# Kernel optimization log

Hardware: AMD Instinct MI355X
Metric: run time of the kernel (lower is better)

## Reference

```python
import jax, jax.numpy as jnp
import numpy as np

B, T, D_MODEL, D_HIDDEN = 4, 8192, 1024, 1024
EPS = 1e-5

def setup_inputs() -> dict:
    key = jax.random.key(0)
    ks = jax.random.split(key, 8)
    s_in = 1.0 / np.sqrt(D_MODEL)
    s_h = 1.0 / np.sqrt(D_HIDDEN)
    return {
        "x": jax.random.normal(ks[0], (B, T, D_MODEL), jnp.float32),
        "W_ih": jax.random.uniform(ks[1], (D_MODEL, D_HIDDEN), jnp.float32, -s_in, s_in),
        "b_ih": jnp.zeros((D_HIDDEN,), jnp.float32),
        "W_gate": jax.random.uniform(ks[2], (D_MODEL, D_HIDDEN), jnp.float32, -s_in, s_in),
        "b_gate": jnp.zeros((D_HIDDEN,), jnp.float32),
        "log_a": jnp.full((D_HIDDEN,), -0.1, jnp.float32),
        "ln_g": jnp.ones((D_HIDDEN,), jnp.float32),
        "ln_b": jnp.zeros((D_HIDDEN,), jnp.float32),
        "W_out": jax.random.uniform(ks[3], (D_HIDDEN, D_HIDDEN), jnp.float32, -s_h, s_h),
        "b_out": jnp.zeros((D_HIDDEN,), jnp.float32),
        "W_proj": jax.random.uniform(ks[4], (D_HIDDEN, D_MODEL), jnp.float32, -s_h, s_h),
        "b_proj": jnp.zeros((D_MODEL,), jnp.float32),
    }

def _scan(alpha, beta):
    # h_t = alpha_t * h_{t-1} + beta_t, h_0 = 0, over axis 1 (time)
    def combine(c1, c2):
        a1, b1 = c1
        a2, b2 = c2
        return a2 * a1, a2 * b1 + b2
    _, h = jax.lax.associative_scan(combine, (alpha, beta), axis=1)
    return h

def reference(x, W_ih, b_ih, W_gate, b_gate, log_a, ln_g, ln_b, W_out, b_out, W_proj, b_proj):
    ih = jnp.einsum("btd,dh->bth", x, W_ih) + b_ih
    gate = jax.nn.sigmoid(jnp.einsum("btd,dh->bth", x, W_gate) + b_gate)
    a = jnp.exp(log_a)  # [H]
    alpha = (1.0 - gate) * a  # [B,T,H]
    beta = gate * ih
    h = _scan(alpha, beta)
    # LayerNorm over last dim
    mu = jnp.mean(h, axis=-1, keepdims=True)
    var = jnp.var(h, axis=-1, keepdims=True)
    hn = (h - mu) * jax.lax.rsqrt(var + EPS) * ln_g + ln_b
    out = jnp.einsum("bth,ho->bto", hn, W_out) + b_out
    return jnp.einsum("bth,hd->btd", out, W_proj) + b_proj
```

## Files before the change

kernel.cpp:

```cpp
#include <hip/hip_runtime.h>

typedef short bhalf8 __attribute__((ext_vector_type(8)));
typedef float floatx4 __attribute__((ext_vector_type(4)));
typedef unsigned short ushortx8 __attribute__((ext_vector_type(8)));

__device__ __forceinline__ unsigned short f2bf(float f){
  union { float f; unsigned int u; } v; v.f = f;
  unsigned int u = v.u;
  u += 0x7fffu + ((u >> 16) & 1u);
  return (unsigned short)(u >> 16);
}
__device__ __forceinline__ float bf2f(unsigned short u){
  union { unsigned int u; float f; } v; v.u = ((unsigned)u) << 16; return v.f;
}
__device__ __forceinline__ unsigned pack2(float a, float b){
  return (unsigned)f2bf(a) | ((unsigned)f2bf(b) << 16);
}

__device__ __forceinline__ void async16(const unsigned short* g, unsigned short* l){
  __builtin_amdgcn_global_load_lds(
      (const __attribute__((address_space(1))) void*)g,
      (__attribute__((address_space(3))) void*)l,
      16, 0, 0);
}

template<int EPI>
__global__ __launch_bounds__(256) void gemm_k(
    const unsigned short* __restrict__ Ab, const unsigned short* __restrict__ BT,
    const float* __restrict__ bias, float* __restrict__ Cf,
    unsigned short* __restrict__ Cb, int K, int ldc)
{
  __shared__ __align__(16) unsigned short As[128*64];
  __shared__ __align__(16) unsigned short Bs[128*64];
  const int tid = threadIdx.x;
  const int n0 = blockIdx.x * 128;
  const int m0 = blockIdx.y * 128;
  const int wid = tid >> 6, lane = tid & 63;
  const int wr = (wid >> 1) * 64, wc = (wid & 1) * 64;
  const int r16 = lane & 15, quad = lane >> 4;
  const int ldsbase = (tid & ~63) * 8;

  const unsigned short* pA[4];
  const unsigned short* pB[4];
  #pragma unroll
  for (int i = 0; i < 4; ++i) {
    int p = tid + i*256;
    int row = p >> 3;
    int cp = (p & 7) ^ (row & 7);
    pA[i] = Ab + (size_t)(m0+row)*K + cp*8;
    pB[i] = BT + (size_t)(n0+row)*K + cp*8;
  }
  int aoff[2][4], boff[2][4];
  #pragma unroll
  for (int ks = 0; ks < 2; ++ks){
    #pragma unroll
    for (int mi = 0; mi < 4; ++mi){
      int row = wr + mi*16 + r16;
      aoff[ks][mi] = (row*8 + ((ks*4+quad) ^ (row&7))) * 8;
    }
    #pragma unroll
    for (int ni = 0; ni < 4; ++ni){
      int row = wc + ni*16 + r16;
      boff[ks][ni] = (row*8 + ((ks*4+quad) ^ (row&7))) * 8;
    }
  }

  floatx4 acc[4][4];
  #pragma unroll
  for (int i=0;i<4;i++)
    #pragma unroll
    for (int j2=0;j2<4;j2++) acc[i][j2] = {0.f,0.f,0.f,0.f};

  for (int k0 = 0; k0 < K; k0 += 64) {
    #pragma unroll
    for (int i = 0; i < 4; ++i) async16(pA[i], &As[ldsbase + i*2048]);
    #pragma unroll
    for (int i = 0; i < 4; ++i) async16(pB[i], &Bs[ldsbase + i*2048]);
    __syncthreads();
    #pragma unroll
    for (int ks = 0; ks < 2; ++ks) {
      bhalf8 aF[4], bF[4];
      #pragma unroll
      for (int mi=0;mi<4;++mi) aF[mi] = *(const bhalf8*)&As[aoff[ks][mi]];
      #pragma unroll
      for (int ni=0;ni<4;++ni) bF[ni] = *(const bhalf8*)&Bs[boff[ks][ni]];
      #pragma unroll
      for (int mi=0;mi<4;++mi)
        #pragma unroll
        for (int ni=0;ni<4;++ni)
          acc[mi][ni] = __builtin_amdgcn_mfma_f32_16x16x32_bf16(aF[mi], bF[ni], acc[mi][ni], 0, 0, 0);
    }
    __syncthreads();
    #pragma unroll
    for (int i = 0; i < 4; ++i) { pA[i] += 64; pB[i] += 64; }
  }

  #pragma unroll
  for (int mi=0;mi<4;++mi)
    #pragma unroll
    for (int ni=0;ni<4;++ni)
      #pragma unroll
      for (int rr=0;rr<4;++rr){
        int m = m0 + wr + mi*16 + quad*4 + rr;
        int n = n0 + wc + ni*16 + r16;
        float val = acc[mi][ni][rr];
        if (EPI == 0) Cf[(size_t)m*ldc + n] = val;
        else if (EPI == 1) Cf[(size_t)m*ldc + n] = val + bias[n];
        else if (EPI == 3) Cb[(size_t)m*ldc + n] = f2bf(val + bias[n]);
        else Cb[(size_t)n*ldc + m] = f2bf(val);
      }
}

__global__ __launch_bounds__(256) void prep_all(
    const float* __restrict__ W_ih, const float* __restrict__ W_gate,
    const float* __restrict__ W_proj, const float* __restrict__ W_out,
    const float* __restrict__ b_out,
    const float* __restrict__ log_a, const float* __restrict__ b_ih,
    const float* __restrict__ b_gate, const float* __restrict__ x,
    unsigned short* __restrict__ WcatT, unsigned short* __restrict__ WprojT,
    unsigned short* __restrict__ Woutb, unsigned short* __restrict__ xb,
    float* __restrict__ Pc, float* __restrict__ a_vec, float* __restrict__ bcat)
{
  __shared__ float tile[32][33];
  const int blk = blockIdx.x;
  const int tid = threadIdx.x;
  if (blk < 3072) {
    const int which = blk >> 10;
    const int t = blk & 1023;
    const float* src = (which == 0) ? W_ih : (which == 1) ? W_gate : W_proj;
    unsigned short* dst = (which == 0) ? WcatT : (which == 1) ? (WcatT + 1024*1024) : WprojT;
    const int c0 = (t & 31) * 32, r0 = (t >> 5) * 32;
    const int tx = tid & 31, ty = tid >> 5;
    #pragma unroll
    for (int i = 0; i < 32; i += 8)
      tile[ty+i][tx] = src[(size_t)(r0+ty+i)*1024 + c0+tx];
    __syncthreads();
    #pragma unroll
    for (int i = 0; i < 32; i += 8)
      dst[(size_t)(c0+ty+i)*1024 + r0+tx] = f2bf(tile[tx][ty+i]);
  } else if (blk < 4096) {
    int idx = ((blk - 3072)*256 + tid) * 4;
    float4 v = *(const float4*)(W_out + idx);
    uint2 p;
    p.x = pack2(v.x, v.y);
    p.y = pack2(v.z, v.w);
    *(uint2*)(Woutb + idx) = p;
  } else if (blk < 4160) {
    int blk2 = blk - 4096;
    int dgrp = blk2 >> 4, seg = blk2 & 15;
    int d = dgrp*256 + tid;
    int e0 = seg*64;
    float acc = 0.f;
    #pragma unroll 8
    for (int e = 0; e < 64; ++e)
      acc += b_out[e0+e] * W_proj[(size_t)(e0+e)*1024 + d];
    Pc[seg*1024 + d] = acc;
  } else if (blk < 4168) {
    int d = (blk - 4160)*256 + tid;
    if (d < 1024) {
      a_vec[d] = __expf(log_a[d]);
      bcat[d] = b_ih[d];
    } else {
      bcat[d] = b_gate[d-1024];
    }
  } else {
    int idx = ((blk - 4168)*256 + tid) * 4;
    float4 v = *(const float4*)(x + idx);
    uint2 p;
    p.x = pack2(v.x, v.y);
    p.y = pack2(v.z, v.w);
    *(uint2*)(xb + idx) = p;
  }
}

#define CHUNK 16
#define NCHUNK 512

__device__ __forceinline__ void ab_step(unsigned short iu, unsigned short gu,
                                        float a, float& al, float& be)
{
  float zi = bf2f(iu), zg = bf2f(gu);
  float g = 1.f / (1.f + __expf(-zg));
  al = (1.f - g) * a;
  be = g * zi;
}

__global__ __launch_bounds__(256, 4) void scan_phase1(const unsigned short* __restrict__ pre,
    const float* __restrict__ a_vec, float* __restrict__ AsT, float* __restrict__ SsT)
{
  __shared__ float sA[4][1024];
  __shared__ float sS[4][1024];
  int wid = threadIdx.x >> 6, lane = threadIdx.x & 63;
  int u = blockIdx.x*4 + wid;
  int b = u >> 9, c = u & (NCHUNK-1);
  int ch0 = lane*16;
  float a[16], A[16], S[16];
  #pragma unroll
  for (int q=0;q<4;++q) *(float4*)&a[q*4] = *(const float4*)(a_vec + ch0 + q*4);
  #pragma unroll
  for (int j=0;j<16;++j){ A[j]=1.f; S[j]=0.f; }
  size_t base = ((size_t)(b*8192 + c*CHUNK))*2048 + ch0;
  for (int t=0;t<CHUNK;++t){
    ushortx8 i0 = *(const ushortx8*)(pre + base);
    ushortx8 i1 = *(const ushortx8*)(pre + base + 8);
    ushortx8 g0 = *(const ushortx8*)(pre + base + 1024);
    ushortx8 g1 = *(const ushortx8*)(pre + base + 1032);
    #pragma unroll
    for (int j=0;j<8;++j){
      float al, be;
      ab_step(i0[j], g0[j], a[j], al, be);
      A[j] *= al; S[j] = al*S[j] + be;
      ab_step(i1[j], g1[j], a[j+8], al, be);
      A[j+8] *= al; S[j+8] = al*S[j+8] + be;
    }
    base += 2048;
  }
  #pragma unroll
  for (int j=0;j<16;++j){ sA[wid][ch0+j] = A[j]; sS[wid][ch0+j] = S[j]; }
  __syncthreads();
  const int bb = blockIdx.x >> 7;
  const int c0 = (blockIdx.x*4) & (NCHUNK-1);
  const int t = threadIdx.x;
  #pragma unroll
  for (int q=0;q<4;++q){
    int ch = t + q*256;
    float4 va = make_float4(sA[0][ch], sA[1][ch], sA[2][ch], sA[3][ch]);
    float4 vs = make_float4(sS[0][ch], sS[1][ch], sS[2][ch], sS[3][ch]);
    size_t o = ((size_t)(bb*1024 + ch))*NCHUNK + c0;
    *(float4*)(AsT + o) = va;
    *(float4*)(SsT + o) = vs;
  }
}

__global__ __launch_bounds__(256) void scan_phase2(const float* __restrict__ AsT,
    const float* __restrict__ SsT, float* __restrict__ carryT,
    const float* __restrict__ Pc, const float* __restrict__ b_proj,
    float* __restrict__ b_comb)
{
  int wid = threadIdx.x >> 6, lane = threadIdx.x & 63;
  int p = blockIdx.x*4 + wid;
  size_t base = (size_t)p*NCHUNK + lane*8;
  float4 a0 = *(const float4*)(AsT + base);
  float4 a1 = *(const float4*)(AsT + base + 4);
  float4 s0 = *(const float4*)(SsT + base);
  float4 s1 = *(const float4*)(SsT + base + 4);
  float A = a0.x, S = s0.x;
  A = a0.y*A; S = a0.y*S + s0.y;
  A = a0.z*A; S = a0.z*S + s0.z;
  A = a0.w*A; S = a0.w*S + s0.w;
  A = a1.x*A; S = a1.x*S + s1.x;
  A = a1.y*A; S = a1.y*S + s1.y;
  A = a1.z*A; S = a1.z*S + s1.z;
  A = a1.w*A; S = a1.w*S + s1.w;
  float iA = A, iS = S;
  #pragma unroll
  for (int d = 1; d < 64; d <<= 1) {
    float pA = __shfl_up(iA, d);
    float pS = __shfl_up(iS, d);
    if (lane >= d) { iS = iA*pS + iS; iA = iA*pA; }
  }
  float bS = __shfl_up(iS, 1);
  if (lane == 0) bS = 0.f;
  float4 c0v, c1v;
  c0v.x = bS; bS = a0.x*bS + s0.x;
  c0v.y = bS; bS = a0.y*bS + s0.y;
  c0v.z = bS; bS = a0.z*bS + s0.z;
  c0v.w = bS; bS = a0.w*bS + s0.w;
  c1v.x = bS; bS = a1.x*bS + s1.x;
  c1v.y = bS; bS = a1.y*bS + s1.y;
  c1v.z = bS; bS = a1.z*bS + s1.z;
  c1v.w = bS;
  *(float4*)(carryT + base)     = c0v;
  *(float4*)(carryT + base + 4) = c1v;

  if (blockIdx.x == 0) {
    #pragma unroll
    for (int q = 0; q < 4; ++q) {
      int d = threadIdx.x + q*256;
      float acc = b_proj[d];
      #pragma unroll
      for (int s = 0; s < 16; ++s) acc += Pc[s*1024 + d];
      b_comb[d] = acc;
    }
  }
}

__global__ __launch_bounds__(256, 4) void scan_phase3(const unsigned short* __restrict__ pre,
    const float* __restrict__ a_vec, const float* __restrict__ carryT,
    const float* __restrict__ ln_g, const float* __restrict__ ln_b,
    unsigned short* __restrict__ hn)
{
  int wid = threadIdx.x >> 6, lane = threadIdx.x & 63;
  int u = blockIdx.x*4 + wid;
  int b = u >> 9, c = u & (NCHUNK-1);
  int ch0 = lane*16;
  float a[16], h[16], g[16], lb[16];
  #pragma unroll
  for (int q=0;q<4;++q){
    *(float4*)&a[q*4]  = *(const float4*)(a_vec + ch0 + q*4);
    *(float4*)&g[q*4]  = *(const float4*)(ln_g + ch0 + q*4);
    *(float4*)&lb[q*4] = *(const float4*)(ln_b + ch0 + q*4);
  }
  #pragma unroll
  for (int j=0;j<16;++j)
    h[j] = carryT[((size_t)b*1024 + ch0 + j)*NCHUNK + c];
  size_t base  = ((size_t)(b*8192 + c*CHUNK))*2048 + ch0;
  size_t hbase = ((size_t)(b*8192 + c*CHUNK))*1024 + ch0;
  for (int t=0;t<CHUNK;++t){
    ushortx8 i0 = *(const ushortx8*)(pre + base);
    ushortx8 i1 = *(const ushortx8*)(pre + base + 8);
    ushortx8 g0 = *(const ushortx8*)(pre + base + 1024);
    ushortx8 g1 = *(const ushortx8*)(pre + base + 1032);
    float s = 0.f, s2 = 0.f;
    #pragma unroll
    for (int j=0;j<8;++j){
      float al, be;
      ab_step(i0[j], g0[j], a[j], al, be);
      h[j] = al*h[j] + be;
      s += h[j]; s2 += h[j]*h[j];
      ab_step(i1[j], g1[j], a[j+8], al, be);
      h[j+8] = al*h[j+8] + be;
      s += h[j+8]; s2 += h[j+8]*h[j+8];
    }
    #pragma unroll
    for (int off = 32; off > 0; off >>= 1) {
      s  += __shfl_xor(s,  off);
      s2 += __shfl_xor(s2, off);
    }
    float mu = s * (1.f/1024.f);
    float var = s2 * (1.f/1024.f) - mu*mu;
    float rstd = rsqrtf(var + 1e-5f);
    uint4 o0, o1;
    float v0, v1;
    v0 = (h[0]-mu)*rstd*g[0]+lb[0];  v1 = (h[1]-mu)*rstd*g[1]+lb[1];  o0.x = pack2(v0,v1);
    v0 = (h[2]-mu)*rstd*g[2]+lb[2];  v1 = (h[3]-mu)*rstd*g[3]+lb[3];  o0.y = pack2(v0,v1);
    v0 = (h[4]-mu)*rstd*g[4]+lb[4];  v1 = (h[5]-mu)*rstd*g[5]+lb[5];  o0.z = pack2(v0,v1);
    v0 = (h[6]-mu)*rstd*g[6]+lb[6];  v1 = (h[7]-mu)*rstd*g[7]+lb[7];  o0.w = pack2(v0,v1);
    v0 = (h[8]-mu)*rstd*g[8]+lb[8];  v1 = (h[9]-mu)*rstd*g[9]+lb[9];  o1.x = pack2(v0,v1);
    v0 = (h[10]-mu)*rstd*g[10]+lb[10]; v1 = (h[11]-mu)*rstd*g[11]+lb[11]; o1.y = pack2(v0,v1);
    v0 = (h[12]-mu)*rstd*g[12]+lb[12]; v1 = (h[13]-mu)*rstd*g[13]+lb[13]; o1.z = pack2(v0,v1);
    v0 = (h[14]-mu)*rstd*g[14]+lb[14]; v1 = (h[15]-mu)*rstd*g[15]+lb[15]; o1.w = pack2(v0,v1);
    *(uint4*)(hn + hbase)     = o0;
    *(uint4*)(hn + hbase + 8) = o1;
    base += 2048; hbase += 1024;
  }
}

extern "C" void kernel_launch(void* const* d_in, const int* in_sizes, int n_in,
                              void* d_out, int out_size, void* d_ws, size_t ws_size,
                              hipStream_t stream)
{
  const float* x      = (const float*)d_in[0];
  const float* W_ih   = (const float*)d_in[1];
  const float* b_ih   = (const float*)d_in[2];
  const float* W_gate = (const float*)d_in[3];
  const float* b_gate = (const float*)d_in[4];
  const float* log_a  = (const float*)d_in[5];
  const float* ln_g   = (const float*)d_in[6];
  const float* ln_b   = (const float*)d_in[7];
  const float* W_out  = (const float*)d_in[8];
  const float* b_out  = (const float*)d_in[9];
  const float* W_proj = (const float*)d_in[10];
  const float* b_proj = (const float*)d_in[11];
  float* out = (float*)d_out;

  char* ws = (char*)d_ws;
  size_t off = 0;
  auto alloc = [&](size_t bytes)->char* {
    char* p = ws + off; off += (bytes + 255) & ~(size_t)255; return p;
  };
  unsigned short* pre   = (unsigned short*)alloc((size_t)32768*2048*2);
  unsigned short* hn    = (unsigned short*)alloc((size_t)32768*1024*2);
  unsigned short* xb    = hn;
  unsigned short* WcatT = (unsigned short*)alloc((size_t)2048*1024*2);
  unsigned short* WprojT= (unsigned short*)alloc((size_t)1024*1024*2);
  unsigned short* Woutb = (unsigned short*)alloc((size_t)1024*1024*2);
  unsigned short* WcombT= (unsigned short*)alloc((size_t)1024*1024*2);
  float* AsT            = (float*)alloc((size_t)4*1024*NCHUNK*4);
  float* SsT            = (float*)alloc((size_t)4*1024*NCHUNK*4);
  float* carryT         = (float*)alloc((size_t)4*1024*NCHUNK*4);
  float* Pc             = (float*)alloc((size_t)16*1024*4);
  float* b_comb         = (float*)alloc(1024*4);
  float* a_vec          = (float*)alloc(1024*4);
  float* bcat           = (float*)alloc(2048*4);

  prep_all<<<4168 + 32768, 256, 0, stream>>>(W_ih, W_gate, W_proj, W_out, b_out,
                                             log_a, b_ih, b_gate, x,
                                             WcatT, WprojT, Woutb, xb,
                                             Pc, a_vec, bcat);
  gemm_k<2><<<dim3(8,8), 256, 0, stream>>>(Woutb, WprojT, nullptr, nullptr, WcombT, 1024, 1024);
  gemm_k<3><<<dim3(16,256), 256, 0, stream>>>(xb, WcatT, bcat, nullptr, pre, 1024, 2048);
  scan_phase1<<<512, 256, 0, stream>>>(pre, a_vec, AsT, SsT);
  scan_phase2<<<1024, 256, 0, stream>>>(AsT, SsT, carryT, Pc, b_proj, b_comb);
  scan_phase3<<<512, 256, 0, stream>>>(pre, a_vec, carryT, ln_g, ln_b, hn);
  gemm_k<1><<<dim3(8,256), 256, 0, stream>>>(hn, WcombT, b_comb, out, nullptr, 1024, 1024);
}
```

Before: 618.5 us.

## Swap MFMA operands for vectorized GEMM epilogue, simplify address math, transpose carry layout

For the bias epilogues, the GEMM passes the MFMA operands in swapped order so each lane holds four consecutive output columns. This allows float4 and packed bf16x4 stores and float4 bias loads in place of scalar strided stores. LDS and global address computation is collapsed into a base offset plus XOR with the k-step, which reduces register pressure. The scan carry buffer is changed to a time-major layout so phase3 reads each carry with contiguous float4 loads instead of 16 strided scalar loads, while phase2 now issues strided scalar stores.

```diff
diff --git a/kernel.cpp b/kernel.cpp
--- a/kernel.cpp
+++ b/kernel.cpp
@@ -40,30 +40,15 @@
   const int r16 = lane & 15, quad = lane >> 4;
   const int ldsbase = (tid & ~63) * 8;
 
-  const unsigned short* pA[4];
-  const unsigned short* pB[4];
-  #pragma unroll
-  for (int i = 0; i < 4; ++i) {
-    int p = tid + i*256;
-    int row = p >> 3;
-    int cp = (p & 7) ^ (row & 7);
-    pA[i] = Ab + (size_t)(m0+row)*K + cp*8;
-    pB[i] = BT + (size_t)(n0+row)*K + cp*8;
-  }
-  int aoff[2][4], boff[2][4];
-  #pragma unroll
-  for (int ks = 0; ks < 2; ++ks){
-    #pragma unroll
-    for (int mi = 0; mi < 4; ++mi){
-      int row = wr + mi*16 + r16;
-      aoff[ks][mi] = (row*8 + ((ks*4+quad) ^ (row&7))) * 8;
-    }
-    #pragma unroll
-    for (int ni = 0; ni < 4; ++ni){
-      int row = wc + ni*16 + r16;
-      boff[ks][ni] = (row*8 + ((ks*4+quad) ^ (row&7))) * 8;
-    }
-  }
+  const int row0 = tid >> 3;
+  const int cp0  = (tid & 7) ^ (row0 & 7);
+  const unsigned short* pA0 = Ab + (size_t)(m0+row0)*K + cp0*8;
+  const unsigned short* pB0 = BT + (size_t)(n0+row0)*K + cp0*8;
+  const size_t slotStride = (size_t)32*K;
+
+  const int swz = quad ^ (r16 & 7);
+  const int abase = ((wr + r16)*8 + swz)*8;
+  const int bbase = ((wc + r16)*8 + swz)*8;
 
   floatx4 acc[4][4];
   #pragma unroll
@@ -73,42 +58,69 @@
 
   for (int k0 = 0; k0 < K; k0 += 64) {
     #pragma unroll
-    for (int i = 0; i < 4; ++i) async16(pA[i], &As[ldsbase + i*2048]);
-    #pragma unroll
-    for (int i = 0; i < 4; ++i) async16(pB[i], &Bs[ldsbase + i*2048]);
+    for (int i = 0; i < 4; ++i) async16(pA0 + i*slotStride, &As[ldsbase + i*2048]);
+    #pragma unroll
+    for (int i = 0; i < 4; ++i) async16(pB0 + i*slotStride, &Bs[ldsbase + i*2048]);
     __syncthreads();
     #pragma unroll
     for (int ks = 0; ks < 2; ++ks) {
+      const int kx = ks*32;
       bhalf8 aF[4], bF[4];
       #pragma unroll
-      for (int mi=0;mi<4;++mi) aF[mi] = *(const bhalf8*)&As[aoff[ks][mi]];
-      #pragma unroll
-      for (int ni=0;ni<4;++ni) bF[ni] = *(const bhalf8*)&Bs[boff[ks][ni]];
+      for (int mi=0;mi<4;++mi) aF[mi] = *(const bhalf8*)&As[(abase + mi*1024) ^ kx];
+      #pragma unroll
+      for (int ni=0;ni<4;++ni) bF[ni] = *(const bhalf8*)&Bs[(bbase + ni*1024) ^ kx];
       #pragma unroll
       for (int mi=0;mi<4;++mi)
         #pragma unroll
-        for (int ni=0;ni<4;++ni)
-          acc[mi][ni] = __builtin_amdgcn_mfma_f32_16x16x32_bf16(aF[mi], bF[ni], acc[mi][ni], 0, 0, 0);
+        for (int ni=0;ni<4;++ni){
+          if (EPI == 1 || EPI == 3)
+            acc[mi][ni] = __builtin_amdgcn_mfma_f32_16x16x32_bf16(bF[ni], aF[mi], acc[mi][ni], 0, 0, 0);
+          else
+            acc[mi][ni] = __builtin_amdgcn_mfma_f32_16x16x32_bf16(aF[mi], bF[ni], acc[mi][ni], 0, 0, 0);
+        }
     }
     __syncthreads();
-    #pragma unroll
-    for (int i = 0; i < 4; ++i) { pA[i] += 64; pB[i] += 64; }
-  }
-
-  #pragma unroll
-  for (int mi=0;mi<4;++mi)
-    #pragma unroll
-    for (int ni=0;ni<4;++ni)
-      #pragma unroll
-      for (int rr=0;rr<4;++rr){
-        int m = m0 + wr + mi*16 + quad*4 + rr;
-        int n = n0 + wc + ni*16 + r16;
-        float val = acc[mi][ni][rr];
-        if (EPI == 0) Cf[(size_t)m*ldc + n] = val;
-        else if (EPI == 1) Cf[(size_t)m*ldc + n] = val + bias[n];
-        else if (EPI == 3) Cb[(size_t)m*ldc + n] = f2bf(val + bias[n]);
-        else Cb[(size_t)n*ldc + m] = f2bf(val);
+    pA0 += 64; pB0 += 64;
+  }
+
+  if (EPI == 1 || EPI == 3) {
+    #pragma unroll
+    for (int mi=0;mi<4;++mi){
+      const int m = m0 + wr + mi*16 + r16;
+      #pragma unroll
+      for (int ni=0;ni<4;++ni){
+        const int n = n0 + wc + ni*16 + quad*4;
+        float4 bv = *(const float4*)&bias[n];
+        float v0 = acc[mi][ni][0] + bv.x;
+        float v1 = acc[mi][ni][1] + bv.y;
+        float v2 = acc[mi][ni][2] + bv.z;
+        float v3 = acc[mi][ni][3] + bv.w;
+        if (EPI == 1) {
+          float4 st = make_float4(v0, v1, v2, v3);
+          *(float4*)&Cf[(size_t)m*ldc + n] = st;
+        } else {
+          uint2 p;
+          p.x = pack2(v0, v1);
+          p.y = pack2(v2, v3);
+          *(uint2*)&Cb[(size_t)m*ldc + n] = p;
+        }
       }
+    }
+  } else {
+    #pragma unroll
+    for (int mi=0;mi<4;++mi)
+      #pragma unroll
+      for (int ni=0;ni<4;++ni)
+        #pragma unroll
+        for (int rr=0;rr<4;++rr){
+          int m = m0 + wr + mi*16 + quad*4 + rr;
+          int n = n0 + wc + ni*16 + r16;
+          float val = acc[mi][ni][rr];
+          if (EPI == 0) Cf[(size_t)m*ldc + n] = val;
+          else Cb[(size_t)n*ldc + m] = f2bf(val);
+        }
+  }
 }
 
 __global__ __launch_bounds__(256) void prep_all(
@@ -233,7 +245,7 @@
 }
 
 __global__ __launch_bounds__(256) void scan_phase2(const float* __restrict__ AsT,
-    const float* __restrict__ SsT, float* __restrict__ carryT,
+    const float* __restrict__ SsT, float* __restrict__ carry,
     const float* __restrict__ Pc, const float* __restrict__ b_proj,
     float* __restrict__ b_comb)
 {
@@ -261,17 +273,16 @@
   }
   float bS = __shfl_up(iS, 1);
   if (lane == 0) bS = 0.f;
-  float4 c0v, c1v;
-  c0v.x = bS; bS = a0.x*bS + s0.x;
-  c0v.y = bS; bS = a0.y*bS + s0.y;
-  c0v.z = bS; bS = a0.z*bS + s0.z;
-  c0v.w = bS; bS = a0.w*bS + s0.w;
-  c1v.x = bS; bS = a1.x*bS + s1.x;
-  c1v.y = bS; bS = a1.y*bS + s1.y;
-  c1v.z = bS; bS = a1.z*bS + s1.z;
-  c1v.w = bS;
-  *(float4*)(carryT + base)     = c0v;
-  *(float4*)(carryT + base + 4) = c1v;
+  const int b2 = p >> 10, ch = p & 1023;
+  size_t o = ((size_t)b2*NCHUNK + lane*8)*1024 + ch;
+  carry[o] = bS; bS = a0.x*bS + s0.x; o += 1024;
+  carry[o] = bS; bS = a0.y*bS + s0.y; o += 1024;
+  carry[o] = bS; bS = a0.z*bS + s0.z; o += 1024;
+  carry[o] = bS; bS = a0.w*bS + s0.w; o += 1024;
+  carry[o] = bS; bS = a1.x*bS + s1.x; o += 1024;
+  carry[o] = bS; bS = a1.y*bS + s1.y; o += 1024;
+  carry[o] = bS; bS = a1.z*bS + s1.z; o += 1024;
+  carry[o] = bS;
 
   if (blockIdx.x == 0) {
     #pragma unroll
@@ -286,7 +297,7 @@
 }
 
 __global__ __launch_bounds__(256, 4) void scan_phase3(const unsigned short* __restrict__ pre,
-    const float* __restrict__ a_vec, const float* __restrict__ carryT,
+    const float* __restrict__ a_vec, const float* __restrict__ carry,
     const float* __restrict__ ln_g, const float* __restrict__ ln_b,
     unsigned short* __restrict__ hn)
 {
@@ -295,15 +306,14 @@
   int b = u >> 9, c = u & (NCHUNK-1);
   int ch0 = lane*16;
   float a[16], h[16], g[16], lb[16];
+  size_t co = ((size_t)b*NCHUNK + c)*1024 + ch0;
   #pragma unroll
   for (int q=0;q<4;++q){
     *(float4*)&a[q*4]  = *(const float4*)(a_vec + ch0 + q*4);
+    *(float4*)&h[q*4]  = *(const float4*)(carry + co + q*4);
     *(float4*)&g[q*4]  = *(const float4*)(ln_g + ch0 + q*4);
     *(float4*)&lb[q*4] = *(const float4*)(ln_b + ch0 + q*4);
   }
-  #pragma unroll
-  for (int j=0;j<16;++j)
-    h[j] = carryT[((size_t)b*1024 + ch0 + j)*NCHUNK + c];
   size_t base  = ((size_t)(b*8192 + c*CHUNK))*2048 + ch0;
   size_t hbase = ((size_t)(b*8192 + c*CHUNK))*1024 + ch0;
   for (int t=0;t<CHUNK;++t){
@@ -378,7 +388,7 @@
   unsigned short* WcombT= (unsigned short*)alloc((size_t)1024*1024*2);
   float* AsT            = (float*)alloc((size_t)4*1024*NCHUNK*4);
   float* SsT            = (float*)alloc((size_t)4*1024*NCHUNK*4);
-  float* carryT         = (float*)alloc((size_t)4*1024*NCHUNK*4);
+  float* carry          = (float*)alloc((size_t)4*NCHUNK*1024*4);
   float* Pc             = (float*)alloc((size_t)16*1024*4);
   float* b_comb         = (float*)alloc(1024*4);
   float* a_vec          = (float*)alloc(1024*4);
@@ -391,7 +401,7 @@
   gemm_k<2><<<dim3(8,8), 256, 0, stream>>>(Woutb, WprojT, nullptr, nullptr, WcombT, 1024, 1024);
   gemm_k<3><<<dim3(16,256), 256, 0, stream>>>(xb, WcatT, bcat, nullptr, pre, 1024, 2048);
   scan_phase1<<<512, 256, 0, stream>>>(pre, a_vec, AsT, SsT);
-  scan_phase2<<<1024, 256, 0, stream>>>(AsT, SsT, carryT, Pc, b_proj, b_comb);
-  scan_phase3<<<512, 256, 0, stream>>>(pre, a_vec, carryT, ln_g, ln_b, hn);
+  scan_phase2<<<1024, 256, 0, stream>>>(AsT, SsT, carry, Pc, b_proj, b_comb);
+  scan_phase3<<<512, 256, 0, stream>>>(pre, a_vec, carry, ln_g, ln_b, hn);
   gemm_k<1><<<dim3(8,256), 256, 0, stream>>>(hn, WcombT, b_comb, out, nullptr, 1024, 1024);
 }
```

Result: slower. 657.3 us (+6.3%).
